# Performance work log

Hardware: AMD Instinct MI355X
Metric: run time of the kernel (lower is better)

Reference implementation:

```python
import jax, jax.numpy as jnp
import numpy as np

B, S, E, H, F = 8, 1024, 1024, 16, 4096
D = E // H  # head_dim = 64
EPS = 1e-5


def setup_inputs() -> dict:
    key = jax.random.key(0)
    ks = jax.random.split(key, 12)
    s = 0.02
    return {
        "x": jax.random.normal(ks[0], (B, S, E), dtype=jnp.float32),
        # per-head projections (shared across heads), torch stores [out,in]; we use [in,out]
        "Wq": jax.random.normal(ks[1], (D, D), dtype=jnp.float32) * s,
        "Wk": jax.random.normal(ks[2], (D, D), dtype=jnp.float32) * s,
        "Wv": jax.random.normal(ks[3], (D, D), dtype=jnp.float32) * s,
        "Wo": jax.random.normal(ks[4], (E, E), dtype=jnp.float32) * s,
        "bo": jnp.zeros((E,), dtype=jnp.float32),
        "W1": jax.random.normal(ks[5], (E, F), dtype=jnp.float32) * s,
        "b1": jnp.zeros((F,), dtype=jnp.float32),
        "W2": jax.random.normal(ks[6], (F, E), dtype=jnp.float32) * s,
        "b2": jnp.zeros((E,), dtype=jnp.float32),
        "g1": jnp.ones((E,), dtype=jnp.float32),
        "beta1": jnp.zeros((E,), dtype=jnp.float32),
        "g2": jnp.ones((E,), dtype=jnp.float32),
        "beta2": jnp.zeros((E,), dtype=jnp.float32),
    }


def _layer_norm(x, g, b):
    m = jnp.mean(x, axis=-1, keepdims=True)
    v = jnp.mean(jnp.square(x - m), axis=-1, keepdims=True)
    return (x - m) * jax.lax.rsqrt(v + EPS) * g + b


def reference(x, Wq, Wk, Wv, Wo, bo, W1, b1, W2, b2, g1, beta1, g2, beta2):
    b, s, e = x.shape
    # --- attention sublayer (pre-norm) ---
    nx = _layer_norm(x, g1, beta1)
    h = nx.reshape(b, s, H, D)              # [B,S,H,D]
    q = h @ Wq                               # per-head linear, weight shared over heads
    k = h @ Wk
    v = h @ Wv
    energy = jnp.einsum('bqhd,bkhd->bhqk', q, k)  # full [B,H,S,S] scores
    mask = jnp.tril(jnp.ones((s, s), dtype=bool))
    energy = jnp.where(mask, energy, -jnp.inf)
    att = jax.nn.softmax(energy / jnp.sqrt(jnp.float32(e)), axis=-1)  # NOTE: scale by sqrt(embed_dim)
    o = jnp.einsum('bhqk,bkhd->bqhd', att, v).reshape(b, s, e)
    x = x + (o @ Wo + bo)
    # --- MLP sublayer (pre-norm); dropout is identity in eval ---
    nx = _layer_norm(x, g2, beta2)
    x = x + (jax.nn.relu(nx @ W1 + b1) @ W2 + b2)
    return x
```

## Files before the change

kernel.cpp:

```cpp
#include <hip/hip_runtime.h>

typedef unsigned short u16;
typedef __attribute__((ext_vector_type(4))) float f4;
typedef __attribute__((ext_vector_type(8))) short s8v;
typedef __attribute__((ext_vector_type(4))) unsigned short u16x4;

#define DEVINL __device__ __forceinline__

DEVINL float b2f(u16 u) { union { unsigned i; float f; } x; x.i = ((unsigned)u) << 16; return x.f; }
DEVINL u16 f2b(float f) {
  union { float f; unsigned i; } x; x.f = f;
  unsigned r = 0x7FFFu + ((x.i >> 16) & 1u);
  return (u16)((x.i + r) >> 16);
}

#define GLD_LDS16(g, l)                                                        \
  __builtin_amdgcn_global_load_lds((__attribute__((address_space(1))) void*)(g), \
                                   (__attribute__((address_space(3))) void*)(l), 16, 0, 0)

__global__ __launch_bounds__(256) void k_transpose(const float* __restrict__ in,
                                                   u16* __restrict__ out, int R, int C) {
  __shared__ float t[32][33];
  int tx = threadIdx.x & 31, ty = threadIdx.x >> 5;
  int c0 = blockIdx.x * 32, r0 = blockIdx.y * 32;
#pragma unroll
  for (int i = 0; i < 32; i += 8)
    t[ty + i][tx] = in[(long)(r0 + ty + i) * C + (c0 + tx)];
  __syncthreads();
#pragma unroll
  for (int i = 0; i < 32; i += 8)
    out[(long)(c0 + ty + i) * R + (r0 + tx)] = f2b(t[tx][ty + i]);
}

__global__ __launch_bounds__(256) void k_vtrans(const u16* __restrict__ v, u16* __restrict__ vt) {
  __shared__ u16 t[64][72];
  int bh = blockIdx.x, b = bh >> 4, h = bh & 15;
  int s0 = blockIdx.y * 64;
  int tid = threadIdx.x;
#pragma unroll
  for (int p = 0; p < 2; ++p) {
    int idx = p * 256 + tid;
    int sl = idx >> 3, c8 = (idx & 7) * 8;
    *(s8v*)(&t[sl][c8]) = *(const s8v*)(v + (((long)(b * 1024 + s0 + sl) * 16 + h) * 64) + c8);
  }
  __syncthreads();
#pragma unroll
  for (int p = 0; p < 2; ++p) {
    int idx = p * 256 + tid;
    int d = idx >> 3, c8 = (idx & 7) * 8;
    s8v o;
#pragma unroll
    for (int e = 0; e < 8; ++e) o[e] = (short)t[c8 + e][d];
    *(s8v*)(vt + ((long)bh * 64 + d) * 1024 + s0 + c8) = o;
  }
}

__global__ __launch_bounds__(256) void k_layernorm(const float* __restrict__ x,
                                                   const float* __restrict__ g,
                                                   const float* __restrict__ be,
                                                   u16* __restrict__ out) {
  long row = blockIdx.x;
  int tid = threadIdx.x;
  f4 v = ((const f4*)(x + row * 1024))[tid];
  float s = v[0] + v[1] + v[2] + v[3];
  float s2 = v[0] * v[0] + v[1] * v[1] + v[2] * v[2] + v[3] * v[3];
#pragma unroll
  for (int off = 32; off > 0; off >>= 1) {
    s += __shfl_down(s, off, 64);
    s2 += __shfl_down(s2, off, 64);
  }
  __shared__ float red[8];
  int wv = tid >> 6, ln = tid & 63;
  if (ln == 0) { red[wv] = s; red[4 + wv] = s2; }
  __syncthreads();
  s = red[0] + red[1] + red[2] + red[3];
  s2 = red[4] + red[5] + red[6] + red[7];
  float mean = s * (1.0f / 1024.0f);
  float var = s2 * (1.0f / 1024.0f) - mean * mean;
  float rs = rsqrtf(var + 1e-5f);
  f4 gg = ((const f4*)g)[tid];
  f4 bb = ((const f4*)be)[tid];
  u16x4 o;
#pragma unroll
  for (int i = 0; i < 4; ++i) o[i] = f2b((v[i] - mean) * rs * gg[i] + bb[i]);
  ((u16x4*)(out + row * 1024))[tid] = o;
}

__global__ __launch_bounds__(256) void k_qkv(const u16* __restrict__ nx, const u16* __restrict__ WqT,
                                             const u16* __restrict__ WkT, const u16* __restrict__ WvT,
                                             u16* __restrict__ q, u16* __restrict__ k,
                                             u16* __restrict__ v) {
  int tid = threadIdx.x, lane = tid & 63, wave = tid >> 6;
  int quad = lane >> 4, l16 = lane & 15;
  long rbase = (long)blockIdx.x * 64 + wave * 16;
  s8v a0 = *(const s8v*)(nx + (rbase + l16) * 64 + quad * 8);
  s8v a1 = *(const s8v*)(nx + (rbase + l16) * 64 + 32 + quad * 8);
  const u16* Ws[3] = {WqT, WkT, WvT};
  u16* Os[3] = {q, k, v};
#pragma unroll
  for (int t = 0; t < 3; ++t) {
#pragma unroll
    for (int j = 0; j < 4; ++j) {
      s8v b0 = *(const s8v*)(Ws[t] + (j * 16 + l16) * 64 + quad * 8);
      s8v b1 = *(const s8v*)(Ws[t] + (j * 16 + l16) * 64 + 32 + quad * 8);
      f4 acc = {0.f, 0.f, 0.f, 0.f};
      acc = __builtin_amdgcn_mfma_f32_16x16x32_bf16(a0, b0, acc, 0, 0, 0);
      acc = __builtin_amdgcn_mfma_f32_16x16x32_bf16(a1, b1, acc, 0, 0, 0);
#pragma unroll
      for (int r = 0; r < 4; ++r)
        Os[t][(rbase + quad * 4 + r) * 64 + j * 16 + l16] = f2b(acc[r]);
    }
  }
}

__global__ __launch_bounds__(256) void k_attn_mfma(const u16* __restrict__ q,
                                                   const u16* __restrict__ kk,
                                                   const u16* __restrict__ vt,
                                                   u16* __restrict__ o) {
  constexpr int LDK = 72;
  __shared__ u16 Ks[64 * LDK];
  __shared__ u16 Vt[64 * LDK];
  __shared__ u16 Ps[4][16 * LDK];
  int tid = threadIdx.x, lane = tid & 63, wave = tid >> 6;
  int quad = lane >> 4, l16 = lane & 15;
  int b = blockIdx.x >> 4, h = blockIdx.x & 15;
  int qi = (int)gridDim.y - 1 - (int)blockIdx.y;
  int q0 = qi * 64 + wave * 16;

  const u16* qp = q + (((long)(b * 1024 + q0 + l16)) * 16 + h) * 64;
  s8v aq0 = *(const s8v*)(qp + quad * 8);
  s8v aq1 = *(const s8v*)(qp + 32 + quad * 8);

  f4 O[4];
  float m_[4], l_[4];
#pragma unroll
  for (int jd = 0; jd < 4; ++jd) O[jd] = f4{0.f, 0.f, 0.f, 0.f};
#pragma unroll
  for (int r = 0; r < 4; ++r) { m_[r] = -__builtin_inff(); l_[r] = 0.f; }

  for (int kt = 0; kt <= qi; ++kt) {
    __syncthreads();
#pragma unroll
    for (int p = 0; p < 2; ++p) {
      int idx = p * 256 + tid;
      int row = idx >> 3, c8 = (idx & 7) * 8;
      *(s8v*)(Ks + row * LDK + c8) =
          *(const s8v*)(kk + (((long)(b * 1024 + kt * 64 + row)) * 16 + h) * 64 + c8);
      *(s8v*)(Vt + row * LDK + c8) =
          *(const s8v*)(vt + ((long)blockIdx.x * 64 + row) * 1024 + kt * 64 + c8);
    }
    __syncthreads();

    f4 sf[4];
#pragma unroll
    for (int jn = 0; jn < 4; ++jn) {
      s8v b0 = *(const s8v*)(Ks + (jn * 16 + l16) * LDK + quad * 8);
      s8v b1 = *(const s8v*)(Ks + (jn * 16 + l16) * LDK + 32 + quad * 8);
      f4 acc = f4{0.f, 0.f, 0.f, 0.f};
      acc = __builtin_amdgcn_mfma_f32_16x16x32_bf16(aq0, b0, acc, 0, 0, 0);
      acc = __builtin_amdgcn_mfma_f32_16x16x32_bf16(aq1, b1, acc, 0, 0, 0);
      sf[jn] = acc;
    }
    bool diag = (kt == qi);
    float rm[4];
#pragma unroll
    for (int r = 0; r < 4; ++r) rm[r] = -__builtin_inff();
#pragma unroll
    for (int jn = 0; jn < 4; ++jn)
#pragma unroll
      for (int r = 0; r < 4; ++r) {
        float v = sf[jn][r] * 0.03125f;
        if (diag && (jn * 16 + l16 > wave * 16 + quad * 4 + r)) v = -__builtin_inff();
        sf[jn][r] = v;
        rm[r] = fmaxf(rm[r], v);
      }
#pragma unroll
    for (int off = 1; off < 16; off <<= 1)
#pragma unroll
      for (int r = 0; r < 4; ++r) rm[r] = fmaxf(rm[r], __shfl_xor(rm[r], off, 64));
    float alpha[4], rs[4];
#pragma unroll
    for (int r = 0; r < 4; ++r) {
      float mn = fmaxf(m_[r], rm[r]);
      alpha[r] = __expf(m_[r] - mn);
      m_[r] = mn;
      rs[r] = 0.f;
    }
#pragma unroll
    for (int jn = 0; jn < 4; ++jn)
#pragma unroll
      for (int r = 0; r < 4; ++r) {
        float p = __expf(sf[jn][r] - m_[r]);
        rs[r] += p;
        Ps[wave][(quad * 4 + r) * LDK + jn * 16 + l16] = f2b(p);
      }
#pragma unroll
    for (int off = 1; off < 16; off <<= 1)
#pragma unroll
      for (int r = 0; r < 4; ++r) rs[r] += __shfl_xor(rs[r], off, 64);
#pragma unroll
    for (int r = 0; r < 4; ++r) l_[r] = l_[r] * alpha[r] + rs[r];
#pragma unroll
    for (int jd = 0; jd < 4; ++jd)
#pragma unroll
      for (int r = 0; r < 4; ++r) O[jd][r] *= alpha[r];
    asm volatile("s_waitcnt lgkmcnt(0)" ::: "memory");
    s8v p0 = *(const s8v*)(&Ps[wave][l16 * LDK + quad * 8]);
    s8v p1 = *(const s8v*)(&Ps[wave][l16 * LDK + 32 + quad * 8]);
#pragma unroll
    for (int jd = 0; jd < 4; ++jd) {
      s8v b0 = *(const s8v*)(Vt + (jd * 16 + l16) * LDK + quad * 8);
      s8v b1 = *(const s8v*)(Vt + (jd * 16 + l16) * LDK + 32 + quad * 8);
      O[jd] = __builtin_amdgcn_mfma_f32_16x16x32_bf16(p0, b0, O[jd], 0, 0, 0);
      O[jd] = __builtin_amdgcn_mfma_f32_16x16x32_bf16(p1, b1, O[jd], 0, 0, 0);
    }
  }
#pragma unroll
  for (int r = 0; r < 4; ++r) {
    float inv = 1.0f / l_[r];
    u16* op = o + (((long)(b * 1024 + q0 + quad * 4 + r)) * 16 + h) * 64;
#pragma unroll
    for (int jd = 0; jd < 4; ++jd) op[jd * 16 + l16] = f2b(O[jd][r] * inv);
  }
}

template <int EPI>
__global__ __launch_bounds__(512) void k_gemm256(const u16* __restrict__ A,
                                                 const u16* __restrict__ BT,
                                                 const float* __restrict__ bias,
                                                 const float* __restrict__ resid,
                                                 void* __restrict__ outp, int M, int N, int K,
                                                 int lda) {
  __shared__ __align__(16) u16 S[65536];
  int tid = threadIdx.x, lane = tid & 63, wave = tid >> 6;
  int l16 = lane & 15, quad = lane >> 4;
  int wm = wave >> 2, wn = wave & 3;
  long bm = blockIdx.x, bn = blockIdx.y;
  int z = blockIdx.z;

  int rl = l16 & 7;
  int c0 = 8 * (quad ^ rl);
  int c1 = 8 * ((quad ^ 4) ^ rl);
  int rowA = (wm * 64 + l16) * 64;
  int rowB = (wn * 32 + l16) * 64;

  int Lb = tid * 16;
  int Ls = Lb ^ (((Lb >> 7) & 7) << 4);
  int r_ = Ls >> 7, kin = (Ls & 127) >> 1;
  const u16* pA = A + (bm * 256 + r_) * (long)lda + kin + (long)z * K;
  const u16* pB = BT + (bn * 256 + r_) * (long)lda + kin + (long)z * K;

  f4 acc[4][4][2];
#pragma unroll
  for (int q = 0; q < 4; ++q)
#pragma unroll
    for (int mi = 0; mi < 4; ++mi)
#pragma unroll
      for (int nj = 0; nj < 2; ++nj) acc[q][mi][nj] = f4{0.f, 0.f, 0.f, 0.f};
  s8v aF[4][2], bF[2][2][2];

#define BAR asm volatile("s_barrier" ::: "memory")
#define LGK0 asm volatile("s_waitcnt lgkmcnt(0)" ::: "memory")
#define WVM4 asm volatile("s_waitcnt vmcnt(4)" ::: "memory")
#define WVM0 asm volatile("s_waitcnt vmcnt(0)" ::: "memory")

#define STAGE(mat, half, t, buf)                                               \
  do {                                                                         \
    const u16* g_ = ((mat) ? pB : pA) + (long)(half) * 128 * lda + (t) * 64;   \
    char* l_ = ((char*)S) + ((buf) * 32768 + (mat) * 16384 + (half) * 8192) * 2 + wave * 1024; \
    GLD_LDS16(g_, l_);                                                         \
    GLD_LDS16(g_ + 64 * (long)lda, l_ + 8192);                                 \
  } while (0)

#define LDA(buf, mh)                                                           \
  do {                                                                         \
    const u16* p_ = S + (buf) * 32768 + (mh) * 8192 + rowA;                    \
    _Pragma("unroll") for (int mi = 0; mi < 4; ++mi) {                         \
      aF[mi][0] = *(const s8v*)(p_ + mi * 1024 + c0);                          \
      aF[mi][1] = *(const s8v*)(p_ + mi * 1024 + c1);                          \
    }                                                                          \
  } while (0)

#define LDB(buf, nh, set)                                                      \
  do {                                                                         \
    const u16* p_ = S + (buf) * 32768 + 16384 + (nh) * 8192 + rowB;            \
    _Pragma("unroll") for (int nj = 0; nj < 2; ++nj) {                         \
      bF[set][nj][0] = *(const s8v*)(p_ + nj * 1024 + c0);                     \
      bF[set][nj][1] = *(const s8v*)(p_ + nj * 1024 + c1);                     \
    }                                                                          \
  } while (0)

#define MM(q)                                                                  \
  do {                                                                         \
    _Pragma("unroll") for (int mi = 0; mi < 4; ++mi)                           \
        _Pragma("unroll") for (int nj = 0; nj < 2; ++nj) {                     \
      acc[q][mi][nj] = __builtin_amdgcn_mfma_f32_16x16x32_bf16(                \
          aF[mi][0], bF[(q) & 1][nj][0], acc[q][mi][nj], 0, 0, 0);             \
      acc[q][mi][nj] = __builtin_amdgcn_mfma_f32_16x16x32_bf16(                \
          aF[mi][1], bF[(q) & 1][nj][1], acc[q][mi][nj], 0, 0, 0);             \
    }                                                                          \
  } while (0)

#define PHASES(t, LAST)                                                        \
  LDA(0, 0); LDB(0, 0, 0); STAGE(0, 1, (t) + 1, 1);                            \
  BAR; LGK0; __builtin_amdgcn_s_setprio(1); MM(0); __builtin_amdgcn_s_setprio(0); BAR; \
  LDB(0, 1, 1); STAGE(1, 1, (t) + 1, 1);                                       \
  BAR; LGK0; __builtin_amdgcn_s_setprio(1); MM(1); __builtin_amdgcn_s_setprio(0); BAR; \
  LDA(0, 1); if (!(LAST)) STAGE(0, 0, (t) + 2, 0);                             \
  BAR; LGK0; __builtin_amdgcn_s_setprio(1); MM(2); __builtin_amdgcn_s_setprio(0); BAR; \
  if (!(LAST)) STAGE(1, 0, (t) + 2, 0);                                        \
  __builtin_amdgcn_s_setprio(1); MM(3); __builtin_amdgcn_s_setprio(0);         \
  if (LAST) { WVM0; } else { WVM4; }                                           \
  BAR;                                                                         \
  LDA(1, 0); LDB(1, 0, 0); if (!(LAST)) STAGE(0, 1, (t) + 2, 0);               \
  BAR; LGK0; __builtin_amdgcn_s_setprio(1); MM(0); __builtin_amdgcn_s_setprio(0); BAR; \
  LDB(1, 1, 1); if (!(LAST)) STAGE(1, 1, (t) + 2, 0);                          \
  BAR; LGK0; __builtin_amdgcn_s_setprio(1); MM(1); __builtin_amdgcn_s_setprio(0); BAR; \
  LDA(1, 1); if (!(LAST)) STAGE(0, 0, (t) + 3, 1);                             \
  BAR; LGK0; __builtin_amdgcn_s_setprio(1); MM(2); __builtin_amdgcn_s_setprio(0); BAR; \
  if (!(LAST)) STAGE(1, 0, (t) + 3, 1);                                        \
  __builtin_amdgcn_s_setprio(1); MM(3); __builtin_amdgcn_s_setprio(0);         \
  if (!(LAST)) { WVM4; BAR; }

  STAGE(0, 0, 0, 0);
  STAGE(1, 0, 0, 0);
  STAGE(0, 1, 0, 0);
  STAGE(1, 1, 0, 0);
  STAGE(0, 0, 1, 1);
  STAGE(1, 0, 1, 1);
  WVM4; BAR;

  int NI = K >> 7;
  for (int i = 0; i < NI - 1; ++i) {
    int t = 2 * i;
    PHASES(t, 0);
  }
  {
    int t = 2 * (NI - 1);
    PHASES(t, 1);
  }

#undef PHASES
#undef MM
#undef LDB
#undef LDA
#undef STAGE
#undef WVM0
#undef WVM4
#undef LGK0
#undef BAR

  float* P0 = (EPI == 0) ? ((float*)outp + (long)z * M * N) : nullptr;
#pragma unroll
  for (int q = 0; q < 4; ++q) {
    int mh = q >> 1, nh = q & 1;
#pragma unroll
    for (int mi = 0; mi < 4; ++mi) {
#pragma unroll
      for (int nj = 0; nj < 2; ++nj) {
        long row = bm * 256 + mh * 128 + wm * 64 + mi * 16 + quad * 4;
        int col = (int)bn * 256 + nh * 128 + wn * 32 + nj * 16 + l16;
        float bcol = 0.f;
        if (EPI != 0) bcol = bias[col];
#pragma unroll
        for (int rr = 0; rr < 4; ++rr) {
          float val = acc[q][mi][nj][rr] + bcol;
          if (EPI == 0) {
            P0[(row + rr) * (long)N + col] = val;
          } else if (EPI == 1) {
            ((u16*)outp)[(row + rr) * (long)N + col] = f2b(val > 0.f ? val : 0.f);
          } else {
            ((float*)outp)[(row + rr) * (long)N + col] =
                resid[(row + rr) * (long)N + col] + val;
          }
        }
      }
    }
  }
}

__global__ __launch_bounds__(512) void k_gemm256n128(const u16* __restrict__ A,
                                                     const u16* __restrict__ BT,
                                                     const float* __restrict__ bias,
                                                     const float* __restrict__ resid,
                                                     float* __restrict__ outp,
                                                     int M, int N, int K, int lda) {
  __shared__ __align__(16) u16 S[49152];
  int tid = threadIdx.x, lane = tid & 63, wave = tid >> 6;
  int l16 = lane & 15, quad = lane >> 4;
  int wm = wave >> 1, wn = wave & 1;
  long bm = blockIdx.x, bn = blockIdx.y;

  int rl = l16 & 7;
  int c0 = 8 * (quad ^ rl);
  int c1 = 8 * ((quad ^ 4) ^ rl);
  int rowA = (wm >> 1) * 8192 + ((wm & 1) * 64 + l16) * 64;
  int rowB = 16384 + (wn * 64 + l16) * 64;

  int Lb = tid * 16;
  int Ls = Lb ^ (((Lb >> 7) & 7) << 4);
  int r_ = Ls >> 7, kin = (Ls & 127) >> 1;
  const u16* pA = A + (bm * 256 + r_) * (long)lda + kin;
  const u16* pB = BT + (bn * 128 + r_) * (long)lda + kin;

  f4 acc[4][4];
#pragma unroll
  for (int mi = 0; mi < 4; ++mi)
#pragma unroll
    for (int nj = 0; nj < 4; ++nj) acc[mi][nj] = f4{0.f, 0.f, 0.f, 0.f};
  s8v aF[4][2], bF[2][2];

#define BAR asm volatile("s_barrier" ::: "memory")
#define LGK0 asm volatile("s_waitcnt lgkmcnt(0)" ::: "memory")
#define WVM4 asm volatile("s_waitcnt vmcnt(4)" ::: "memory")
#define WVM0 asm volatile("s_waitcnt vmcnt(0)" ::: "memory")

#define STAGEA(t, buf)                                                         \
  do {                                                                         \
    const u16* g_ = pA + (t) * 64;                                             \
    char* l_ = ((char*)S) + (buf) * 49152 + wave * 1024;                       \
    GLD_LDS16(g_, l_);                                                         \
    GLD_LDS16(g_ + 64 * (long)lda, l_ + 8192);                                 \
    GLD_LDS16(g_ + 128 * (long)lda, l_ + 16384);                               \
    GLD_LDS16(g_ + 192 * (long)lda, l_ + 24576);                               \
  } while (0)

#define STAGEB(t, buf)                                                         \
  do {                                                                         \
    const u16* g_ = pB + (t) * 64;                                             \
    char* l_ = ((char*)S) + (buf) * 49152 + 32768 + wave * 1024;               \
    GLD_LDS16(g_, l_);                                                         \
    GLD_LDS16(g_ + 64 * (long)lda, l_ + 8192);                                 \
  } while (0)

#define LDAn(buf)                                                              \
  do {                                                                         \
    const u16* p_ = S + (buf) * 24576 + rowA;                                  \
    _Pragma("unroll") for (int mi = 0; mi < 4; ++mi) {                         \
      aF[mi][0] = *(const s8v*)(p_ + mi * 1024 + c0);                          \
      aF[mi][1] = *(const s8v*)(p_ + mi * 1024 + c1);                          \
    }                                                                          \
  } while (0)

#define LDBn(buf, nh)                                                          \
  do {                                                                         \
    const u16* p_ = S + (buf) * 24576 + rowB + (nh) * 2048;                    \
    _Pragma("unroll") for (int nj2 = 0; nj2 < 2; ++nj2) {                      \
      bF[nj2][0] = *(const s8v*)(p_ + nj2 * 1024 + c0);                        \
      bF[nj2][1] = *(const s8v*)(p_ + nj2 * 1024 + c1);                        \
    }                                                                          \
  } while (0)

#define MMn(nh)                                                                \
  do {                                                                         \
    _Pragma("unroll") for (int mi = 0; mi < 4; ++mi)                           \
        _Pragma("unroll") for (int nj2 = 0; nj2 < 2; ++nj2) {                  \
      acc[mi][(nh) * 2 + nj2] = __builtin_amdgcn_mfma_f32_16x16x32_bf16(       \
          aF[mi][0], bF[nj2][0], acc[mi][(nh) * 2 + nj2], 0, 0, 0);            \
      acc[mi][(nh) * 2 + nj2] = __builtin_amdgcn_mfma_f32_16x16x32_bf16(       \
          aF[mi][1], bF[nj2][1], acc[mi][(nh) * 2 + nj2], 0, 0, 0);            \
    }                                                                          \
  } while (0)

#define PHASES(t, LAST)                                                        \
                                                                      \
  LDAn(0); LDBn(0, 0); STAGEB((t) + 1, 1);                                     \
  BAR; LGK0; __builtin_amdgcn_s_setprio(1); MMn(0); __builtin_amdgcn_s_setprio(0); BAR; \
                                                                      \
  LDBn(0, 1); if (!(LAST)) STAGEA((t) + 2, 0);                                 \
  BAR; LGK0; __builtin_amdgcn_s_setprio(1); MMn(1); __builtin_amdgcn_s_setprio(0); \
  if (LAST) { WVM0; } else { WVM4; }                                           \
  BAR;                                                                         \
                                                                      \
  LDAn(1); LDBn(1, 0); if (!(LAST)) STAGEB((t) + 2, 0);                        \
  BAR; LGK0; __builtin_amdgcn_s_setprio(1); MMn(0); __builtin_amdgcn_s_setprio(0); BAR; \
                                                                      \
  LDBn(1, 1); if (!(LAST)) STAGEA((t) + 3, 1);                                 \
  BAR; LGK0; __builtin_amdgcn_s_setprio(1); MMn(1); __builtin_amdgcn_s_setprio(0); \
  if (!(LAST)) { WVM4; }                                                       \
  BAR;

  STAGEA(0, 0);
  STAGEB(0, 0);
  STAGEA(1, 1);
  WVM4; BAR;

  int NI = K >> 7;
  for (int i = 0; i < NI - 1; ++i) {
    int t = 2 * i;
    PHASES(t, 0);
  }
  {
    int t = 2 * (NI - 1);
    PHASES(t, 1);
  }

#undef PHASES
#undef MMn
#undef LDBn
#undef LDAn
#undef STAGEB
#undef STAGEA
#undef WVM0
#undef WVM4
#undef LGK0
#undef BAR

#pragma unroll
  for (int mi = 0; mi < 4; ++mi) {
#pragma unroll
    for (int nj = 0; nj < 4; ++nj) {
      long row = bm * 256 + wm * 64 + mi * 16 + quad * 4;
      int col = (int)bn * 128 + wn * 64 + nj * 16 + l16;
      float bcol = bias[col];
#pragma unroll
      for (int rr = 0; rr < 4; ++rr) {
        outp[(row + rr) * (long)N + col] =
            resid[(row + rr) * (long)N + col] + acc[mi][nj][rr] + bcol;
      }
    }
  }
}

extern "C" void kernel_launch(void* const* d_in, const int* in_sizes, int n_in, void* d_out,
                              int out_size, void* d_ws, size_t ws_size, hipStream_t stream) {
  const float* x = (const float*)d_in[0];
  const float* Wq = (const float*)d_in[1];
  const float* Wk = (const float*)d_in[2];
  const float* Wv = (const float*)d_in[3];
  const float* Wo = (const float*)d_in[4];
  const float* bo = (const float*)d_in[5];
  const float* W1 = (const float*)d_in[6];
  const float* b1 = (const float*)d_in[7];
  const float* W2 = (const float*)d_in[8];
  const float* b2 = (const float*)d_in[9];
  const float* g1 = (const float*)d_in[10];
  const float* be1 = (const float*)d_in[11];
  const float* g2 = (const float*)d_in[12];
  const float* be2 = (const float*)d_in[13];

  char* ws = (char*)d_ws;
  const size_t MB = 1ull << 20;
  u16* nx = (u16*)(ws + 0);
  u16* qb = (u16*)(ws + 16 * MB);
  u16* kb = (u16*)(ws + 32 * MB);
  u16* vb = (u16*)(ws + 48 * MB);
  float* x1 = (float*)(ws + 64 * MB);
  u16* h1 = (u16*)(ws + 96 * MB);
  u16* vtr = (u16*)(ws + 96 * MB);
  u16* WoT = (u16*)(ws + 160 * MB);
  u16* W1T = (u16*)(ws + 162 * MB);
  u16* W2T = (u16*)(ws + 170 * MB);
  u16* WqT = (u16*)(ws + 178 * MB);
  u16* WkT = WqT + 64 * 64;
  u16* WvT = WkT + 64 * 64;
  u16* ob = nx;
  u16* nx2 = qb;

  k_transpose<<<dim3(32, 32), 256, 0, stream>>>(Wo, WoT, 1024, 1024);
  k_transpose<<<dim3(128, 32), 256, 0, stream>>>(W1, W1T, 1024, 4096);
  k_transpose<<<dim3(32, 128), 256, 0, stream>>>(W2, W2T, 4096, 1024);
  k_transpose<<<dim3(2, 2), 256, 0, stream>>>(Wq, WqT, 64, 64);
  k_transpose<<<dim3(2, 2), 256, 0, stream>>>(Wk, WkT, 64, 64);
  k_transpose<<<dim3(2, 2), 256, 0, stream>>>(Wv, WvT, 64, 64);

  k_layernorm<<<8192, 256, 0, stream>>>(x, g1, be1, nx);
  k_qkv<<<2048, 256, 0, stream>>>(nx, WqT, WkT, WvT, qb, kb, vb);
  k_vtrans<<<dim3(128, 16), 256, 0, stream>>>(vb, vtr);
  k_attn_mfma<<<dim3(128, 16), 256, 0, stream>>>(qb, kb, vtr, ob);
  k_gemm256n128<<<dim3(32, 8), 512, 0, stream>>>(ob, WoT, bo, x, x1, 8192, 1024, 1024, 1024);

  k_layernorm<<<8192, 256, 0, stream>>>(x1, g2, be2, nx2);
  k_gemm256<1><<<dim3(32, 16, 1), 512, 0, stream>>>(nx2, W1T, b1, nullptr, h1, 8192, 4096, 1024, 1024);
  k_gemm256n128<<<dim3(32, 8), 512, 0, stream>>>(h1, W2T, b2, x1, (float*)d_out, 8192, 1024, 4096, 4096);
}
```

Before: 414.9 us.

## Remap GEMM workgroups across XCDs, batch small transposes, prioritize attention MFMA

Both GEMM kernels now remap the linear workgroup id so that consecutive ids dispatched round-robin to the 8 XCDs own contiguous tile regions, which should improve L2 reuse of the A and B tiles. The three 64x64 weight transposes are merged into one launch with a z dimension, saving two kernel launches. The attention kernel raises wave priority around its MFMA sections with s_setprio. The remap assumes the grid size is divisible by 8, and the priority hints may have little effect.

```diff
diff --git a/kernel.cpp b/kernel.cpp
--- a/kernel.cpp
+++ b/kernel.cpp
@@ -30,6 +30,25 @@
 #pragma unroll
   for (int i = 0; i < 32; i += 8)
     out[(long)(c0 + ty + i) * R + (r0 + tx)] = f2b(t[tx][ty + i]);
+}
+
+__global__ __launch_bounds__(256) void k_transpose3(const float* __restrict__ i0,
+                                                    const float* __restrict__ i1,
+                                                    const float* __restrict__ i2,
+                                                    u16* __restrict__ o0, u16* __restrict__ o1,
+                                                    u16* __restrict__ o2) {
+  const float* in = blockIdx.z == 0 ? i0 : (blockIdx.z == 1 ? i1 : i2);
+  u16* out = blockIdx.z == 0 ? o0 : (blockIdx.z == 1 ? o1 : o2);
+  __shared__ float t[32][33];
+  int tx = threadIdx.x & 31, ty = threadIdx.x >> 5;
+  int c0 = blockIdx.x * 32, r0 = blockIdx.y * 32;
+#pragma unroll
+  for (int i = 0; i < 32; i += 8)
+    t[ty + i][tx] = in[(long)(r0 + ty + i) * 64 + (c0 + tx)];
+  __syncthreads();
+#pragma unroll
+  for (int i = 0; i < 32; i += 8)
+    out[(long)(c0 + ty + i) * 64 + (r0 + tx)] = f2b(t[tx][ty + i]);
 }
 
 __global__ __launch_bounds__(256) void k_vtrans(const u16* __restrict__ v, u16* __restrict__ vt) {
@@ -152,6 +171,7 @@
     __syncthreads();
 
     f4 sf[4];
+    __builtin_amdgcn_s_setprio(1);
 #pragma unroll
     for (int jn = 0; jn < 4; ++jn) {
       s8v b0 = *(const s8v*)(Ks + (jn * 16 + l16) * LDK + quad * 8);
@@ -161,6 +181,7 @@
       acc = __builtin_amdgcn_mfma_f32_16x16x32_bf16(aq1, b1, acc, 0, 0, 0);
       sf[jn] = acc;
     }
+    __builtin_amdgcn_s_setprio(0);
     bool diag = (kt == qi);
     float rm[4];
 #pragma unroll
@@ -207,6 +228,7 @@
     asm volatile("s_waitcnt lgkmcnt(0)" ::: "memory");
     s8v p0 = *(const s8v*)(&Ps[wave][l16 * LDK + quad * 8]);
     s8v p1 = *(const s8v*)(&Ps[wave][l16 * LDK + 32 + quad * 8]);
+    __builtin_amdgcn_s_setprio(1);
 #pragma unroll
     for (int jd = 0; jd < 4; ++jd) {
       s8v b0 = *(const s8v*)(Vt + (jd * 16 + l16) * LDK + quad * 8);
@@ -214,6 +236,7 @@
       O[jd] = __builtin_amdgcn_mfma_f32_16x16x32_bf16(p0, b0, O[jd], 0, 0, 0);
       O[jd] = __builtin_amdgcn_mfma_f32_16x16x32_bf16(p1, b1, O[jd], 0, 0, 0);
     }
+    __builtin_amdgcn_s_setprio(0);
   }
 #pragma unroll
   for (int r = 0; r < 4; ++r) {
@@ -235,7 +258,10 @@
   int tid = threadIdx.x, lane = tid & 63, wave = tid >> 6;
   int l16 = lane & 15, quad = lane >> 4;
   int wm = wave >> 2, wn = wave & 3;
-  long bm = blockIdx.x, bn = blockIdx.y;
+  int o_ = blockIdx.y * gridDim.x + blockIdx.x;
+  int nwg_ = gridDim.x * gridDim.y, qq_ = nwg_ >> 3;
+  int lid_ = (o_ & 7) * qq_ + (o_ >> 3);
+  long bm = lid_ % gridDim.x, bn = lid_ / gridDim.x;
   int z = blockIdx.z;
 
   int rl = l16 & 7;
@@ -389,7 +415,10 @@
   int tid = threadIdx.x, lane = tid & 63, wave = tid >> 6;
   int l16 = lane & 15, quad = lane >> 4;
   int wm = wave >> 1, wn = wave & 1;
-  long bm = blockIdx.x, bn = blockIdx.y;
+  int o_ = blockIdx.y * gridDim.x + blockIdx.x;
+  int nwg_ = gridDim.x * gridDim.y, qq_ = nwg_ >> 3;
+  int lid_ = (o_ & 7) * qq_ + (o_ >> 3);
+  long bm = lid_ % gridDim.x, bn = lid_ / gridDim.x;
 
   int rl = l16 & 7;
   int c0 = 8 * (quad ^ rl);
@@ -463,18 +492,14 @@
   } while (0)
 
 #define PHASES(t, LAST)                                                        \
-                                                                      \
   LDAn(0); LDBn(0, 0); STAGEB((t) + 1, 1);                                     \
   BAR; LGK0; __builtin_amdgcn_s_setprio(1); MMn(0); __builtin_amdgcn_s_setprio(0); BAR; \
-                                                                      \
   LDBn(0, 1); if (!(LAST)) STAGEA((t) + 2, 0);                                 \
   BAR; LGK0; __builtin_amdgcn_s_setprio(1); MMn(1); __builtin_amdgcn_s_setprio(0); \
   if (LAST) { WVM0; } else { WVM4; }                                           \
   BAR;                                                                         \
-                                                                      \
   LDAn(1); LDBn(1, 0); if (!(LAST)) STAGEB((t) + 2, 0);                        \
   BAR; LGK0; __builtin_amdgcn_s_setprio(1); MMn(0); __builtin_amdgcn_s_setprio(0); BAR; \
-                                                                      \
   LDBn(1, 1); if (!(LAST)) STAGEA((t) + 3, 1);                                 \
   BAR; LGK0; __builtin_amdgcn_s_setprio(1); MMn(1); __builtin_amdgcn_s_setprio(0); \
   if (!(LAST)) { WVM4; }                                                       \
@@ -560,9 +585,7 @@
   k_transpose<<<dim3(32, 32), 256, 0, stream>>>(Wo, WoT, 1024, 1024);
   k_transpose<<<dim3(128, 32), 256, 0, stream>>>(W1, W1T, 1024, 4096);
   k_transpose<<<dim3(32, 128), 256, 0, stream>>>(W2, W2T, 4096, 1024);
-  k_transpose<<<dim3(2, 2), 256, 0, stream>>>(Wq, WqT, 64, 64);
-  k_transpose<<<dim3(2, 2), 256, 0, stream>>>(Wk, WkT, 64, 64);
-  k_transpose<<<dim3(2, 2), 256, 0, stream>>>(Wv, WvT, 64, 64);
+  k_transpose3<<<dim3(2, 2, 3), 256, 0, stream>>>(Wq, Wk, Wv, WqT, WkT, WvT);
 
   k_layernorm<<<8192, 256, 0, stream>>>(x, g1, be1, nx);
   k_qkv<<<2048, 256, 0, stream>>>(nx, WqT, WkT, WvT, qb, kb, vb);
```

New measurement: 449.7 us. +8.4%, slower.
